# Optimization experiments

Hardware: AMD Instinct MI355X
Metric: run time of the kernel (lower is better)

Reference implementation:

```python
import jax, jax.numpy as jnp
import numpy as np

B, L, H, E, D = 2, 2048, 8, 64, 64

def setup_inputs() -> dict:
    key = jax.random.key(0)
    kq, kk, kv, ks = jax.random.split(key, 4)
    return {
        "queries": jax.random.normal(kq, (B, L, H, E), dtype=jnp.float32),
        "keys": jax.random.normal(kk, (B, L, H, E), dtype=jnp.float32),
        "values": jax.random.normal(kv, (B, L, H, D), dtype=jnp.float32),
        "sigma": jax.random.normal(ks, (B, L, H), dtype=jnp.float32),
    }

def reference(queries, keys, values, sigma):
    b, l, h, e = queries.shape
    scale = 1.0 / np.sqrt(e).astype(np.float32)
    # raw attention scores [B,H,L,S]
    scores = jnp.einsum('blhe,bshe->bhls', queries, keys)
    # strict causal mask (mask j > i)
    causal = jnp.triu(jnp.ones((l, l), dtype=bool), k=1)
    scores = jnp.where(causal[None, None], -jnp.inf, scores)
    attn = scale * scores
    # learned Gaussian prior per query-key distance
    sig = jnp.transpose(sigma, (0, 2, 1))            # [B,H,L]
    sig = jax.nn.sigmoid(sig * 5.0) + 1e-5
    sig = jnp.power(3.0, sig) - 1.0                  # in (0, 2)
    sig = sig[..., None]                             # [B,H,L,1] broadcast over window
    idx = jnp.arange(l, dtype=jnp.float32)
    dist = jnp.abs(idx[:, None] - idx[None, :])      # [L,L]
    inv_sqrt_2pi = 1.0 / np.sqrt(2.0 * np.pi).astype(np.float32)
    prior = (inv_sqrt_2pi / sig) * jnp.exp(-(dist[None, None] ** 2) / (2.0 * sig ** 2))  # [B,H,L,L]
    series = jax.nn.softmax(attn, axis=-1)           # [B,H,L,S]
    V = jnp.einsum('bhls,bshd->blhd', series, values)  # [B,L,H,D]
    sigma_out = jnp.broadcast_to(sig, prior.shape)
    return V, series, prior, sigma_out
```

## Files before the change

### kernel.cpp

```cpp
#include <hip/hip_runtime.h>

#define L_ 2048
#define H_ 8

typedef __attribute__((ext_vector_type(8))) short short8;
typedef __attribute__((ext_vector_type(4))) float f32x4;

static constexpr size_t OFF_S = 2097152;
static constexpr size_t OFF_P = OFF_S + 67108864;
static constexpr size_t OFF_G = OFF_P + 67108864;

static constexpr size_t WS_K = 1u << 20;
static constexpr size_t WS_V = WS_K + (4u << 20);

__device__ __forceinline__ unsigned short f2bf(float x) {
    union { float f; unsigned int u; } c; c.f = x;
    unsigned int u = c.u;
    u += 0x7fffu + ((u >> 16) & 1u);
    return (unsigned short)(u >> 16);
}

__device__ __forceinline__ void gld_lds16(const unsigned short* g, unsigned short* l) {
    __builtin_amdgcn_global_load_lds(
        (const __attribute__((address_space(1))) void*)g,
        (__attribute__((address_space(3))) void*)l, 16, 0, 0);
}

__device__ __forceinline__ void st_nt4(float* p, f32x4 v) {
    __builtin_nontemporal_store(v, reinterpret_cast<f32x4*>(p));
}
__device__ __forceinline__ void st_nt1(float* p, float v) {
    __builtin_nontemporal_store(v, p);
}

__global__ __launch_bounds__(256) void prep(
    const float* __restrict__ k, const float* __restrict__ v,
    unsigned short* __restrict__ wsK, unsigned short* __restrict__ wsV)
{
    const int tid = threadIdx.x;
    const int blk = blockIdx.x;
    __shared__ __attribute__((aligned(16))) unsigned short tr[64][72];
    if (blk < 512) {
        const int bh = blk >> 5, t = blk & 31;
        const int b = bh >> 3, h = bh & 7;
        unsigned short* dst = wsK + (size_t)(bh * 32 + t) * 4096;
        #pragma unroll
        for (int p = 0; p < 2; ++p) {
            const int cid = tid + (p << 8);
            const int r = cid >> 3, c = cid & 7;
            const int j = (t << 6) + r;
            const float4* src = reinterpret_cast<const float4*>(
                k + (((size_t)((b * L_ + j) * H_ + h)) << 6) + (c << 3));
            float4 x0 = src[0], x1 = src[1];
            union { short8 s; unsigned short u[8]; } w;
            w.u[0]=f2bf(x0.x); w.u[1]=f2bf(x0.y); w.u[2]=f2bf(x0.z); w.u[3]=f2bf(x0.w);
            w.u[4]=f2bf(x1.x); w.u[5]=f2bf(x1.y); w.u[6]=f2bf(x1.z); w.u[7]=f2bf(x1.w);
            *reinterpret_cast<short8*>(dst + r * 64 + ((c ^ (r & 7)) << 3)) = w.s;
        }
    } else {
        const int vb = blk - 512;
        const int bh = vb >> 5, t = vb & 31;
        const int b = bh >> 3, h = bh & 7;
        const int col4 = (tid & 15) << 2;
        #pragma unroll
        for (int p = 0; p < 4; ++p) {
            const int r = (tid >> 4) + (p << 4);
            const int j = (t << 6) + r;
            float4 x = *reinterpret_cast<const float4*>(
                v + (((size_t)((b * L_ + j) * H_ + h)) << 6) + col4);
            tr[col4 + 0][r] = f2bf(x.x); tr[col4 + 1][r] = f2bf(x.y);
            tr[col4 + 2][r] = f2bf(x.z); tr[col4 + 3][r] = f2bf(x.w);
        }
        __syncthreads();
        unsigned short* dst = wsV + (size_t)(bh * 32 + t) * 4096;
        #pragma unroll
        for (int p = 0; p < 2; ++p) {
            const int cid = tid + (p << 8);
            const int d = cid >> 3, cj = cid & 7;
            short8 s = *reinterpret_cast<const short8*>(&tr[d][cj << 3]);
            *reinterpret_cast<short8*>(dst + d * 64 + ((cj ^ (d & 7)) << 3)) = s;
        }
    }
}

__global__ __launch_bounds__(256) void fused(
    const float* __restrict__ q, const float* __restrict__ sg,
    const unsigned short* __restrict__ wsK, const unsigned short* __restrict__ wsV,
    float* __restrict__ out)
{
    __shared__ __attribute__((aligned(16))) unsigned short Kb[2][4096];
    __shared__ __attribute__((aligned(16))) unsigned short Vb[2][4096];
    __shared__ __attribute__((aligned(16))) unsigned short Pt[16][72];
    __shared__ float l_sums[16];
    __shared__ float sA[16], sC2[16], sS[16];

    const int tid  = threadIdx.x;
    const int wv   = tid >> 6;
    const int lane = tid & 63;
    const int quad = lane >> 4;
    const int l16  = lane & 15;

    const int blk = blockIdx.x;
    const int s   = 127 - (blk >> 4);
    const int bh  = blk & 15;
    const int b   = bh >> 3, h = bh & 7;
    const int i0  = s << 4;

    const int ntiles = (s >> 2) + 1;
    const unsigned short* gK = wsK + ((size_t)bh * 32) * 4096;
    const unsigned short* gV = wsV + ((size_t)bh * 32) * 4096;

    #define STAGE(buf, t) do {                                              \
        const unsigned short* _sk = gK + (size_t)(t) * 4096;                \
        const unsigned short* _sv = gV + (size_t)(t) * 4096;                \
        _Pragma("unroll")                                                   \
        for (int _qq = 0; _qq < 2; ++_qq) {                                 \
            const int _off = (wv << 10) + (_qq << 9);                       \
            gld_lds16(_sk + _off + (lane << 3), &Kb[buf][_off]);            \
            gld_lds16(_sv + _off + (lane << 3), &Vb[buf][_off]);            \
        }                                                                   \
    } while (0)

    STAGE(0, 0);

    if (tid < 16) {
        l_sums[tid] = 0.0f;
        const int i = i0 + tid;
        const float x = sg[(size_t)((b * L_ + i) * H_ + h)];
        const float sgm = 1.0f / (1.0f + __expf(-5.0f * x)) + 1e-5f;
        const float sp  = expm1f(sgm * 1.0986122886681098f);
        sS[tid]  = sp;
        sA[tid]  = 0.3989422804014327f / sp;
        sC2[tid] = 0.5f / (sp * sp);
    }

    short8 a0, a1;
    {
        const float* qr = q + (((size_t)((b * L_ + (i0 + l16)) * H_ + h)) << 6);
        const float4* q4 = reinterpret_cast<const float4*>(qr) + quad * 2;
        float4 x0 = q4[0], x1 = q4[1];
        float4 y0 = q4[8], y1 = q4[9];
        union { short8 v8; unsigned short u[8]; } fa, fb;
        fa.u[0]=f2bf(x0.x); fa.u[1]=f2bf(x0.y); fa.u[2]=f2bf(x0.z); fa.u[3]=f2bf(x0.w);
        fa.u[4]=f2bf(x1.x); fa.u[5]=f2bf(x1.y); fa.u[6]=f2bf(x1.z); fa.u[7]=f2bf(x1.w);
        fb.u[0]=f2bf(y0.x); fb.u[1]=f2bf(y0.y); fb.u[2]=f2bf(y0.z); fb.u[3]=f2bf(y0.w);
        fb.u[4]=f2bf(y1.x); fb.u[5]=f2bf(y1.y); fb.u[6]=f2bf(y1.z); fb.u[7]=f2bf(y1.w);
        a0 = fa.v8; a1 = fb.v8;
    }

    f32x4 oacc = {0.f, 0.f, 0.f, 0.f};
    float lpart[4] = {0.f, 0.f, 0.f, 0.f};
    const int r = (wv << 4) + l16;

    for (int t = 0; t < ntiles; ++t) {
        const int p = t & 1;
        __syncthreads();
        if (t + 1 < ntiles) STAGE(1 - p, t + 1);
        short8 b0 = *reinterpret_cast<const short8*>(&Kb[p][r * 64 + ((quad ^ (r & 7)) << 3)]);
        short8 b1 = *reinterpret_cast<const short8*>(&Kb[p][r * 64 + (((quad + 4) ^ (r & 7)) << 3)]);
        f32x4 c4 = {0.f, 0.f, 0.f, 0.f};
        c4 = __builtin_amdgcn_mfma_f32_16x16x32_bf16(a0, b0, c4, 0, 0, 0);
        c4 = __builtin_amdgcn_mfma_f32_16x16x32_bf16(a1, b1, c4, 0, 0, 0);
        const int j = (t << 6) + r;
        #pragma unroll
        for (int rr = 0; rr < 4; ++rr) {
            const int i = i0 + (quad << 2) + rr;
            float pv = (j <= i) ? __expf(c4[rr] * 0.125f - 8.0f) : 0.0f;
            lpart[rr] += pv;
            Pt[(quad << 2) + rr][r] = f2bf(pv);
        }
        __syncthreads();
        short8 pa0 = *reinterpret_cast<const short8*>(&Pt[l16][quad << 3]);
        short8 pa1 = *reinterpret_cast<const short8*>(&Pt[l16][32 + (quad << 3)]);
        short8 vb0 = *reinterpret_cast<const short8*>(&Vb[p][r * 64 + ((quad ^ (r & 7)) << 3)]);
        short8 vb1 = *reinterpret_cast<const short8*>(&Vb[p][r * 64 + (((quad + 4) ^ (r & 7)) << 3)]);
        oacc = __builtin_amdgcn_mfma_f32_16x16x32_bf16(pa0, vb0, oacc, 0, 0, 0);
        oacc = __builtin_amdgcn_mfma_f32_16x16x32_bf16(pa1, vb1, oacc, 0, 0, 0);
    }
    #undef STAGE

    #pragma unroll
    for (int rr = 0; rr < 4; ++rr) {
        float x = lpart[rr];
        x += __shfl_xor(x, 1); x += __shfl_xor(x, 2);
        x += __shfl_xor(x, 4); x += __shfl_xor(x, 8);
        if (l16 == 0) atomicAdd(&l_sums[(quad << 2) + rr], x);
    }
    __syncthreads();

    float inv[4];
    #pragma unroll
    for (int rr = 0; rr < 4; ++rr) inv[rr] = 1.0f / l_sums[(quad << 2) + rr];
    #pragma unroll
    for (int rr = 0; rr < 4; ++rr) {
        const int i = i0 + (quad << 2) + rr;
        st_nt1(out + (((size_t)((b * L_ + i) * H_ + h)) << 6) + (wv << 4) + l16,
               oacc[rr] * inv[rr]);
    }

    float* outS = out + OFF_S;
    float* outP = out + OFF_P;
    float* outG = out + OFF_G;
    float* Ps = reinterpret_cast<float*>(&Kb[0][0]);

    const int rowc = (wv << 2) + quad;
    const int colc = l16 << 2;
    const float Ac  = sA[rowc], C2c = sC2[rowc], Sc = sS[rowc];
    const float fic = (float)(i0 + rowc);
    const size_t rowbase = ((size_t)(bh * L_ + i0 + rowc)) << 11;
    const f32x4 svc = {Sc, Sc, Sc, Sc};

    const int off0 = r * 64 + ((quad ^ (r & 7)) << 3);
    const int off1 = r * 64 + (((quad + 4) ^ (r & 7)) << 3);

    short8 kb0 = *reinterpret_cast<const short8*>(gK + off0);
    short8 kb1 = *reinterpret_cast<const short8*>(gK + off1);
    int t = 0;
    for (; t < ntiles; ++t) {
        short8 kn0 = kb0, kn1 = kb1;
        if (t + 1 < ntiles) {
            const unsigned short* kp = gK + (((size_t)(t + 1)) << 12);
            kn0 = *reinterpret_cast<const short8*>(kp + off0);
            kn1 = *reinterpret_cast<const short8*>(kp + off1);
        }
        f32x4 c4 = {0.f, 0.f, 0.f, 0.f};
        c4 = __builtin_amdgcn_mfma_f32_16x16x32_bf16(a0, kb0, c4, 0, 0, 0);
        c4 = __builtin_amdgcn_mfma_f32_16x16x32_bf16(a1, kb1, c4, 0, 0, 0);
        const int j = (t << 6) + r;
        #pragma unroll
        for (int rr = 0; rr < 4; ++rr) {
            const int i = i0 + (quad << 2) + rr;
            const float pv = (j <= i) ? __expf(c4[rr] * 0.125f - 8.0f) * inv[rr] : 0.0f;
            Ps[((quad << 2) + rr) * 68 + r] = pv;
        }
        asm volatile("s_waitcnt lgkmcnt(0)" ::: "memory");
        __builtin_amdgcn_s_barrier();
        asm volatile("" ::: "memory");
        const f32x4 se = *reinterpret_cast<const f32x4*>(&Ps[rowc * 68 + colc]);
        const int c = (t << 6) + colc;
        const float d0 = fic - (float)c;
        const float d1 = d0 - 1.f, d2 = d0 - 2.f, d3 = d0 - 3.f;
        f32x4 pr;
        pr.x = Ac * __expf(-d0 * d0 * C2c);
        pr.y = Ac * __expf(-d1 * d1 * C2c);
        pr.z = Ac * __expf(-d2 * d2 * C2c);
        pr.w = Ac * __expf(-d3 * d3 * C2c);
        st_nt4(outS + rowbase + c, se);
        st_nt4(outP + rowbase + c, pr);
        st_nt4(outG + rowbase + c, svc);
        asm volatile("s_waitcnt lgkmcnt(0)" ::: "memory");
        __builtin_amdgcn_s_barrier();
        asm volatile("" ::: "memory");
        kb0 = kn0; kb1 = kn1;
    }
    const f32x4 z4 = {0.f, 0.f, 0.f, 0.f};
    for (; t < 32; ++t) {
        const int c = (t << 6) + colc;
        const float d0 = fic - (float)c;
        const float d1 = d0 - 1.f, d2 = d0 - 2.f, d3 = d0 - 3.f;
        f32x4 pr;
        pr.x = Ac * __expf(-d0 * d0 * C2c);
        pr.y = Ac * __expf(-d1 * d1 * C2c);
        pr.z = Ac * __expf(-d2 * d2 * C2c);
        pr.w = Ac * __expf(-d3 * d3 * C2c);
        st_nt4(outS + rowbase + c, z4);
        st_nt4(outP + rowbase + c, pr);
        st_nt4(outG + rowbase + c, svc);
    }
}

extern "C" void kernel_launch(void* const* d_in, const int* in_sizes, int n_in,
                              void* d_out, int out_size, void* d_ws, size_t ws_size,
                              hipStream_t stream) {
    const float* q  = (const float*)d_in[0];
    const float* k  = (const float*)d_in[1];
    const float* v  = (const float*)d_in[2];
    const float* sg = (const float*)d_in[3];
    float* outp = (float*)d_out;
    unsigned short* wsK = (unsigned short*)((char*)d_ws + WS_K);
    unsigned short* wsV = (unsigned short*)((char*)d_ws + WS_V);
    prep<<<dim3(1024), dim3(256), 0, stream>>>(k, v, wsK, wsV);
    fused<<<dim3(2048), dim3(256), 0, stream>>>(q, sg, wsK, wsV, outp);
}
```

Baseline: 851.7 us.

## Process 32 query rows per block and double-buffer the series staging

Each block now handles 32 query rows instead of 16, so the grid halves and every K/V tile loaded into LDS is reused for two MFMA row groups. The epilogue's series staging now alternates between the K and V LDS buffers, which removes one barrier per tile. Launch bounds request 4 blocks per CU. The costs are more registers per thread and coarser work granularity across the causal triangle. The kernel is dominated by writing roughly 800MB of outputs, so it is likely bandwidth-bound.

```diff
diff --git a/kernel.cpp b/kernel.cpp
--- a/kernel.cpp
+++ b/kernel.cpp
@@ -83,16 +83,16 @@
     }
 }
 
-__global__ __launch_bounds__(256) void fused(
+__global__ __launch_bounds__(256, 4) void fused(
     const float* __restrict__ q, const float* __restrict__ sg,
     const unsigned short* __restrict__ wsK, const unsigned short* __restrict__ wsV,
     float* __restrict__ out)
 {
     __shared__ __attribute__((aligned(16))) unsigned short Kb[2][4096];
     __shared__ __attribute__((aligned(16))) unsigned short Vb[2][4096];
-    __shared__ __attribute__((aligned(16))) unsigned short Pt[16][72];
-    __shared__ float l_sums[16];
-    __shared__ float sA[16], sC2[16], sS[16];
+    __shared__ __attribute__((aligned(16))) unsigned short Pt[32][72];
+    __shared__ float l_sums[32];
+    __shared__ float sA[32], sC2[32], sS[32];
 
     const int tid  = threadIdx.x;
     const int wv   = tid >> 6;
@@ -101,12 +101,12 @@
     const int l16  = lane & 15;
 
     const int blk = blockIdx.x;
-    const int s   = 127 - (blk >> 4);
+    const int s   = 63 - (blk >> 4);
     const int bh  = blk & 15;
     const int b   = bh >> 3, h = bh & 7;
-    const int i0  = s << 4;
-
-    const int ntiles = (s >> 2) + 1;
+    const int i0  = s << 5;
+
+    const int ntiles = (s >> 1) + 1;
     const unsigned short* gK = wsK + ((size_t)bh * 32) * 4096;
     const unsigned short* gV = wsV + ((size_t)bh * 32) * 4096;
 
@@ -123,7 +123,7 @@
 
     STAGE(0, 0);
 
-    if (tid < 16) {
+    if (tid < 32) {
         l_sums[tid] = 0.0f;
         const int i = i0 + tid;
         const float x = sg[(size_t)((b * L_ + i) * H_ + h)];
@@ -134,9 +134,10 @@
         sC2[tid] = 0.5f / (sp * sp);
     }
 
-    short8 a0, a1;
-    {
-        const float* qr = q + (((size_t)((b * L_ + (i0 + l16)) * H_ + h)) << 6);
+    short8 a0[2], a1[2];
+    #pragma unroll
+    for (int qh = 0; qh < 2; ++qh) {
+        const float* qr = q + (((size_t)((b * L_ + (i0 + (qh << 4) + l16)) * H_ + h)) << 6);
         const float4* q4 = reinterpret_cast<const float4*>(qr) + quad * 2;
         float4 x0 = q4[0], x1 = q4[1];
         float4 y0 = q4[8], y1 = q4[9];
@@ -145,11 +146,11 @@
         fa.u[4]=f2bf(x1.x); fa.u[5]=f2bf(x1.y); fa.u[6]=f2bf(x1.z); fa.u[7]=f2bf(x1.w);
         fb.u[0]=f2bf(y0.x); fb.u[1]=f2bf(y0.y); fb.u[2]=f2bf(y0.z); fb.u[3]=f2bf(y0.w);
         fb.u[4]=f2bf(y1.x); fb.u[5]=f2bf(y1.y); fb.u[6]=f2bf(y1.z); fb.u[7]=f2bf(y1.w);
-        a0 = fa.v8; a1 = fb.v8;
-    }
-
-    f32x4 oacc = {0.f, 0.f, 0.f, 0.f};
-    float lpart[4] = {0.f, 0.f, 0.f, 0.f};
+        a0[qh] = fa.v8; a1[qh] = fb.v8;
+    }
+
+    f32x4 oacc[2] = {{0.f,0.f,0.f,0.f}, {0.f,0.f,0.f,0.f}};
+    float lpart[2][4] = {{0.f,0.f,0.f,0.f}, {0.f,0.f,0.f,0.f}};
     const int r = (wv << 4) + l16;
 
     for (int t = 0; t < ntiles; ++t) {
@@ -158,57 +159,75 @@
         if (t + 1 < ntiles) STAGE(1 - p, t + 1);
         short8 b0 = *reinterpret_cast<const short8*>(&Kb[p][r * 64 + ((quad ^ (r & 7)) << 3)]);
         short8 b1 = *reinterpret_cast<const short8*>(&Kb[p][r * 64 + (((quad + 4) ^ (r & 7)) << 3)]);
-        f32x4 c4 = {0.f, 0.f, 0.f, 0.f};
-        c4 = __builtin_amdgcn_mfma_f32_16x16x32_bf16(a0, b0, c4, 0, 0, 0);
-        c4 = __builtin_amdgcn_mfma_f32_16x16x32_bf16(a1, b1, c4, 0, 0, 0);
         const int j = (t << 6) + r;
         #pragma unroll
-        for (int rr = 0; rr < 4; ++rr) {
-            const int i = i0 + (quad << 2) + rr;
-            float pv = (j <= i) ? __expf(c4[rr] * 0.125f - 8.0f) : 0.0f;
-            lpart[rr] += pv;
-            Pt[(quad << 2) + rr][r] = f2bf(pv);
+        for (int qh = 0; qh < 2; ++qh) {
+            f32x4 c4 = {0.f, 0.f, 0.f, 0.f};
+            c4 = __builtin_amdgcn_mfma_f32_16x16x32_bf16(a0[qh], b0, c4, 0, 0, 0);
+            c4 = __builtin_amdgcn_mfma_f32_16x16x32_bf16(a1[qh], b1, c4, 0, 0, 0);
+            #pragma unroll
+            for (int rr = 0; rr < 4; ++rr) {
+                const int i = i0 + (qh << 4) + (quad << 2) + rr;
+                float pv = (j <= i) ? __expf(c4[rr] * 0.125f - 8.0f) : 0.0f;
+                lpart[qh][rr] += pv;
+                Pt[(qh << 4) + (quad << 2) + rr][r] = f2bf(pv);
+            }
         }
         __syncthreads();
-        short8 pa0 = *reinterpret_cast<const short8*>(&Pt[l16][quad << 3]);
-        short8 pa1 = *reinterpret_cast<const short8*>(&Pt[l16][32 + (quad << 3)]);
         short8 vb0 = *reinterpret_cast<const short8*>(&Vb[p][r * 64 + ((quad ^ (r & 7)) << 3)]);
         short8 vb1 = *reinterpret_cast<const short8*>(&Vb[p][r * 64 + (((quad + 4) ^ (r & 7)) << 3)]);
-        oacc = __builtin_amdgcn_mfma_f32_16x16x32_bf16(pa0, vb0, oacc, 0, 0, 0);
-        oacc = __builtin_amdgcn_mfma_f32_16x16x32_bf16(pa1, vb1, oacc, 0, 0, 0);
+        #pragma unroll
+        for (int qh = 0; qh < 2; ++qh) {
+            short8 pa0 = *reinterpret_cast<const short8*>(&Pt[(qh << 4) + l16][quad << 3]);
+            short8 pa1 = *reinterpret_cast<const short8*>(&Pt[(qh << 4) + l16][32 + (quad << 3)]);
+            oacc[qh] = __builtin_amdgcn_mfma_f32_16x16x32_bf16(pa0, vb0, oacc[qh], 0, 0, 0);
+            oacc[qh] = __builtin_amdgcn_mfma_f32_16x16x32_bf16(pa1, vb1, oacc[qh], 0, 0, 0);
+        }
     }
     #undef STAGE
 
     #pragma unroll
+    for (int qh = 0; qh < 2; ++qh)
+    #pragma unroll
     for (int rr = 0; rr < 4; ++rr) {
-        float x = lpart[rr];
+        float x = lpart[qh][rr];
         x += __shfl_xor(x, 1); x += __shfl_xor(x, 2);
         x += __shfl_xor(x, 4); x += __shfl_xor(x, 8);
-        if (l16 == 0) atomicAdd(&l_sums[(quad << 2) + rr], x);
+        if (l16 == 0) atomicAdd(&l_sums[(qh << 4) + (quad << 2) + rr], x);
     }
     __syncthreads();
 
-    float inv[4];
-    #pragma unroll
-    for (int rr = 0; rr < 4; ++rr) inv[rr] = 1.0f / l_sums[(quad << 2) + rr];
+    float inv[2][4];
+    #pragma unroll
+    for (int qh = 0; qh < 2; ++qh)
     #pragma unroll
     for (int rr = 0; rr < 4; ++rr) {
-        const int i = i0 + (quad << 2) + rr;
+        inv[qh][rr] = 1.0f / l_sums[(qh << 4) + (quad << 2) + rr];
+        const int i = i0 + (qh << 4) + (quad << 2) + rr;
         st_nt1(out + (((size_t)((b * L_ + i) * H_ + h)) << 6) + (wv << 4) + l16,
-               oacc[rr] * inv[rr]);
+               oacc[qh][rr] * inv[qh][rr]);
     }
 
     float* outS = out + OFF_S;
     float* outP = out + OFF_P;
     float* outG = out + OFF_G;
-    float* Ps = reinterpret_cast<float*>(&Kb[0][0]);
-
-    const int rowc = (wv << 2) + quad;
+    float* PsA = reinterpret_cast<float*>(&Kb[0][0]);
+    float* PsB = reinterpret_cast<float*>(&Vb[0][0]);
+
+    const int rc0  = (wv << 2) + quad;
     const int colc = l16 << 2;
-    const float Ac  = sA[rowc], C2c = sC2[rowc], Sc = sS[rowc];
-    const float fic = (float)(i0 + rowc);
-    const size_t rowbase = ((size_t)(bh * L_ + i0 + rowc)) << 11;
-    const f32x4 svc = {Sc, Sc, Sc, Sc};
+    float Ac[2], C2c[2], fic[2];
+    f32x4 svc[2];
+    size_t rowbase[2];
+    #pragma unroll
+    for (int ps = 0; ps < 2; ++ps) {
+        const int row = rc0 + (ps << 4);
+        Ac[ps]  = sA[row]; C2c[ps] = sC2[row];
+        const float Sv = sS[row];
+        svc[ps] = (f32x4){Sv, Sv, Sv, Sv};
+        fic[ps] = (float)(i0 + row);
+        rowbase[ps] = ((size_t)(bh * L_ + i0 + row)) << 11;
+    }
 
     const int off0 = r * 64 + ((quad ^ (r & 7)) << 3);
     const int off1 = r * 64 + (((quad + 4) ^ (r & 7)) << 3);
@@ -223,49 +242,56 @@
             kn0 = *reinterpret_cast<const short8*>(kp + off0);
             kn1 = *reinterpret_cast<const short8*>(kp + off1);
         }
-        f32x4 c4 = {0.f, 0.f, 0.f, 0.f};
-        c4 = __builtin_amdgcn_mfma_f32_16x16x32_bf16(a0, kb0, c4, 0, 0, 0);
-        c4 = __builtin_amdgcn_mfma_f32_16x16x32_bf16(a1, kb1, c4, 0, 0, 0);
+        float* Ps = (t & 1) ? PsB : PsA;
         const int j = (t << 6) + r;
         #pragma unroll
-        for (int rr = 0; rr < 4; ++rr) {
-            const int i = i0 + (quad << 2) + rr;
-            const float pv = (j <= i) ? __expf(c4[rr] * 0.125f - 8.0f) * inv[rr] : 0.0f;
-            Ps[((quad << 2) + rr) * 68 + r] = pv;
+        for (int qh = 0; qh < 2; ++qh) {
+            f32x4 c4 = {0.f, 0.f, 0.f, 0.f};
+            c4 = __builtin_amdgcn_mfma_f32_16x16x32_bf16(a0[qh], kb0, c4, 0, 0, 0);
+            c4 = __builtin_amdgcn_mfma_f32_16x16x32_bf16(a1[qh], kb1, c4, 0, 0, 0);
+            #pragma unroll
+            for (int rr = 0; rr < 4; ++rr) {
+                const int i = i0 + (qh << 4) + (quad << 2) + rr;
+                const float pv = (j <= i) ? __expf(c4[rr] * 0.125f - 8.0f) * inv[qh][rr] : 0.0f;
+                Ps[((qh << 4) + (quad << 2) + rr) * 68 + r] = pv;
+            }
         }
         asm volatile("s_waitcnt lgkmcnt(0)" ::: "memory");
+        __builtin_amdgcn_sched_barrier(0);
         __builtin_amdgcn_s_barrier();
-        asm volatile("" ::: "memory");
-        const f32x4 se = *reinterpret_cast<const f32x4*>(&Ps[rowc * 68 + colc]);
-        const int c = (t << 6) + colc;
-        const float d0 = fic - (float)c;
-        const float d1 = d0 - 1.f, d2 = d0 - 2.f, d3 = d0 - 3.f;
-        f32x4 pr;
-        pr.x = Ac * __expf(-d0 * d0 * C2c);
-        pr.y = Ac * __expf(-d1 * d1 * C2c);
-        pr.z = Ac * __expf(-d2 * d2 * C2c);
-        pr.w = Ac * __expf(-d3 * d3 * C2c);
-        st_nt4(outS + rowbase + c, se);
-        st_nt4(outP + rowbase + c, pr);
-        st_nt4(outG + rowbase + c, svc);
-        asm volatile("s_waitcnt lgkmcnt(0)" ::: "memory");
-        __builtin_amdgcn_s_barrier();
-        asm volatile("" ::: "memory");
+        #pragma unroll
+        for (int ps = 0; ps < 2; ++ps) {
+            const f32x4 se = *reinterpret_cast<const f32x4*>(&Ps[(rc0 + (ps << 4)) * 68 + colc]);
+            const int c = (t << 6) + colc;
+            const float d0 = fic[ps] - (float)c;
+            const float d1 = d0 - 1.f, d2 = d0 - 2.f, d3 = d0 - 3.f;
+            f32x4 pr;
+            pr.x = Ac[ps] * __expf(-d0 * d0 * C2c[ps]);
+            pr.y = Ac[ps] * __expf(-d1 * d1 * C2c[ps]);
+            pr.z = Ac[ps] * __expf(-d2 * d2 * C2c[ps]);
+            pr.w = Ac[ps] * __expf(-d3 * d3 * C2c[ps]);
+            st_nt4(outS + rowbase[ps] + c, se);
+            st_nt4(outP + rowbase[ps] + c, pr);
+            st_nt4(outG + rowbase[ps] + c, svc[ps]);
+        }
         kb0 = kn0; kb1 = kn1;
     }
     const f32x4 z4 = {0.f, 0.f, 0.f, 0.f};
     for (; t < 32; ++t) {
-        const int c = (t << 6) + colc;
-        const float d0 = fic - (float)c;
-        const float d1 = d0 - 1.f, d2 = d0 - 2.f, d3 = d0 - 3.f;
-        f32x4 pr;
-        pr.x = Ac * __expf(-d0 * d0 * C2c);
-        pr.y = Ac * __expf(-d1 * d1 * C2c);
-        pr.z = Ac * __expf(-d2 * d2 * C2c);
-        pr.w = Ac * __expf(-d3 * d3 * C2c);
-        st_nt4(outS + rowbase + c, z4);
-        st_nt4(outP + rowbase + c, pr);
-        st_nt4(outG + rowbase + c, svc);
+        #pragma unroll
+        for (int ps = 0; ps < 2; ++ps) {
+            const int c = (t << 6) + colc;
+            const float d0 = fic[ps] - (float)c;
+            const float d1 = d0 - 1.f, d2 = d0 - 2.f, d3 = d0 - 3.f;
+            f32x4 pr;
+            pr.x = Ac[ps] * __expf(-d0 * d0 * C2c[ps]);
+            pr.y = Ac[ps] * __expf(-d1 * d1 * C2c[ps]);
+            pr.z = Ac[ps] * __expf(-d2 * d2 * C2c[ps]);
+            pr.w = Ac[ps] * __expf(-d3 * d3 * C2c[ps]);
+            st_nt4(outS + rowbase[ps] + c, z4);
+            st_nt4(outP + rowbase[ps] + c, pr);
+            st_nt4(outG + rowbase[ps] + c, svc[ps]);
+        }
     }
 }
 
@@ -280,5 +306,5 @@
     unsigned short* wsK = (unsigned short*)((char*)d_ws + WS_K);
     unsigned short* wsV = (unsigned short*)((char*)d_ws + WS_V);
     prep<<<dim3(1024), dim3(256), 0, stream>>>(k, v, wsK, wsV);
-    fused<<<dim3(2048), dim3(256), 0, stream>>>(q, sg, wsK, wsV, outp);
-}
+    fused<<<dim3(1024), dim3(256), 0, stream>>>(q, sg, wsK, wsV, outp);
+}
```

Measured after the change: 852.8 us. No clear change (+0.1%).
